# Optimization experiments

Measured on AMD Instinct MI355X. Metric: run time of the kernel, lower is better.

The kernel has to match this reference:

```python
import jax, jax.numpy as jnp
import numpy as np

T, B, D, H = 128, 64, 1024, 1024

def hard_sigmoid(x):
    # torch: clamp(x + 0.5, 0, 1)
    return jnp.clip(x + 0.5, 0.0, 1.0)

def hard_tanh(x):
    # torch F.hardtanh default: clamp(x, -1, 1)
    return jnp.clip(x, -1.0, 1.0)

def setup_inputs() -> dict:
    key = jax.random.key(0)
    k1, k2, k3 = jax.random.split(key, 3)
    scale = 1.0 / np.sqrt(H)
    x = jax.random.normal(k1, (T, B, D), dtype=jnp.float32)
    Wx = jax.random.normal(k2, (D, 4 * H), dtype=jnp.float32) * scale
    Wh = jax.random.normal(k3, (H, 4 * H), dtype=jnp.float32) * scale
    b = jnp.zeros((4 * H,), dtype=jnp.float32)
    return {"x": x, "Wx": Wx, "Wh": Wh, "b": b}

def reference(x, Wx, Wh, b):
    # Hard-LSTM cell unrolled over time (dim 0), state carried via lax.scan.
    Bsz = x.shape[1]
    Hd = Wh.shape[0]

    def step(carry, xt):
        h, c = carry
        gates = xt @ Wx + h @ Wh + b          # [B, 4H]
        i, f, g, o = jnp.split(gates, 4, axis=-1)
        i = hard_sigmoid(i)
        f = hard_sigmoid(f)
        g = hard_tanh(g)
        o = hard_sigmoid(o)
        c_new = f * c + i * g
        h_new = o * hard_tanh(c_new)
        return (h_new, c_new), h_new

    h0 = jnp.zeros((Bsz, Hd), dtype=x.dtype)
    c0 = jnp.zeros((Bsz, Hd), dtype=x.dtype)
    _, hs = jax.lax.scan(step, (h0, c0), x)   # hs: [T, B, H]
    return hs
```

## Files before the change

### kernel.cpp

```cpp
#include <hip/hip_runtime.h>

#define TT 128
#define BB 64
#define DD 1024
#define HH 1024
#define G4 4096
#define MM (TT*BB)
#define BH (BB*HH)

#define NWG 256

__device__ __forceinline__ float hsig(float x) {
    x += 0.5f;
    return fminf(fmaxf(x, 0.0f), 1.0f);
}
__device__ __forceinline__ float htanh(float x) {
    return fminf(fmaxf(x, -1.0f), 1.0f);
}

__global__ void zero_bar(unsigned* p) {
    p[threadIdx.x] = 0u;
}

__global__ __launch_bounds__(256) void gx_gemm(const float* __restrict__ X,
                                               const float* __restrict__ W,
                                               const float* __restrict__ bias,
                                               float* __restrict__ C) {
    __shared__ float As[16][132];
    __shared__ float Bs[16][132];

    const int tid = threadIdx.x;
    const int tx = tid & 15;
    const int ty = tid >> 4;
    const int m0 = blockIdx.y * 128;
    const int n0 = blockIdx.x * 128;

    float acc[8][8] = {};
    float4 ra[2], rb[2];

    #pragma unroll
    for (int i = 0; i < 2; ++i) {
        int f4 = tid + i * 256;
        ra[i] = *(const float4*)(X + (size_t)(m0 + (f4 >> 2)) * DD + (f4 & 3) * 4);
        rb[i] = *(const float4*)(W + (size_t)(f4 >> 5) * G4 + n0 + (f4 & 31) * 4);
    }

    for (int k0 = 0; k0 < DD; k0 += 16) {
        #pragma unroll
        for (int i = 0; i < 2; ++i) {
            int f4 = tid + i * 256;
            int mi = f4 >> 2, kq = f4 & 3;
            As[kq * 4 + 0][mi] = ra[i].x;
            As[kq * 4 + 1][mi] = ra[i].y;
            As[kq * 4 + 2][mi] = ra[i].z;
            As[kq * 4 + 3][mi] = ra[i].w;
            *(float4*)&Bs[f4 >> 5][(f4 & 31) * 4] = rb[i];
        }
        __syncthreads();

        const int kn = (k0 + 16 < DD) ? (k0 + 16) : k0;
        #pragma unroll
        for (int i = 0; i < 2; ++i) {
            int f4 = tid + i * 256;
            ra[i] = *(const float4*)(X + (size_t)(m0 + (f4 >> 2)) * DD + kn + (f4 & 3) * 4);
            rb[i] = *(const float4*)(W + (size_t)(kn + (f4 >> 5)) * G4 + n0 + (f4 & 31) * 4);
        }

        #pragma unroll
        for (int kk = 0; kk < 16; ++kk) {
            float ar[8], br[8];
            *(float4*)&ar[0] = *(const float4*)&As[kk][ty * 4];
            *(float4*)&ar[4] = *(const float4*)&As[kk][64 + ty * 4];
            *(float4*)&br[0] = *(const float4*)&Bs[kk][tx * 4];
            *(float4*)&br[4] = *(const float4*)&Bs[kk][64 + tx * 4];
            #pragma unroll
            for (int i = 0; i < 8; ++i)
                #pragma unroll
                for (int j = 0; j < 8; ++j)
                    acc[i][j] += ar[i] * br[j];
        }
        __syncthreads();
    }

    float bl[8];
    *(float4*)&bl[0] = *(const float4*)(bias + n0 + tx * 4);
    *(float4*)&bl[4] = *(const float4*)(bias + n0 + 64 + tx * 4);
    #pragma unroll
    for (int i = 0; i < 8; ++i) {
        int mrow = m0 + ty * 4 + (i & 3) + 64 * (i >> 2);
        float* crow = C + (size_t)mrow * G4 + n0;
        float4 o1, o2;
        o1.x = acc[i][0] + bl[0]; o1.y = acc[i][1] + bl[1];
        o1.z = acc[i][2] + bl[2]; o1.w = acc[i][3] + bl[3];
        o2.x = acc[i][4] + bl[4]; o2.y = acc[i][5] + bl[5];
        o2.z = acc[i][6] + bl[6]; o2.w = acc[i][7] + bl[7];
        *(float4*)(crow + tx * 4) = o1;
        *(float4*)(crow + 64 + tx * 4) = o2;
    }
}

__global__ __launch_bounds__(512) void lstm_persist(const float* __restrict__ Gx,
                                                    const float* __restrict__ Wh,
                                                    float* __restrict__ out,
                                                    unsigned* __restrict__ flags) {
    __shared__ float smem[16672];
    float* hs  = smem;
    float* red = smem;

    const int tid = threadIdx.x;
    const int btile = blockIdx.x >> 5;
    const int hct   = blockIdx.x & 31;
    const int b0 = btile * 8;

    const int kc = tid >> 4;
    const int tt = tid & 15;
    const int gate = tt >> 2;
    const int hq8  = (tt & 3) * 8;
    const float* wbase = Wh + (size_t)(kc * 32) * G4 + gate * HH + hct * 32 + hq8;

    const bool cell_act = (tid < 256);
    const int cb   = (tid >> 5) & 7;
    const int chcm = tid & 31;
    const size_t cell_g = (size_t)(b0 + cb) * G4 + hct * 32 + chcm;
    const size_t cell_h = (size_t)(b0 + cb) * HH + hct * 32 + chcm;
    float creg = 0.0f;

    const int half_id = cb >> 2;
    const int ridx = (cb & 3) * 8 + (chcm & 7);

    unsigned* gflags = flags + btile * 32;

    if (cell_act) {
        const float* gr = Gx + cell_g;
        float ii = hsig(gr[0]);
        float gv = htanh(gr[2 * HH]);
        float oo = hsig(gr[3 * HH]);
        creg = ii * gv;
        __hip_atomic_store(out + cell_h, oo * htanh(creg),
                           __ATOMIC_RELAXED, __HIP_MEMORY_SCOPE_AGENT);
    }
    asm volatile("s_waitcnt vmcnt(0)" ::: "memory");
    __syncthreads();
    if (tid == 0)
        __hip_atomic_store(gflags + hct, 1u, __ATOMIC_RELAXED,
                           __HIP_MEMORY_SCOPE_AGENT);

    for (int t = 1; t < TT; ++t) {
        float gi = 0.f, gf = 0.f, gg = 0.f, go = 0.f;
        if (cell_act) {
            const float* gr = Gx + (size_t)t * BB * G4 + cell_g;
            gi = gr[0];
            gf = gr[HH];
            gg = gr[2 * HH];
            go = gr[3 * HH];
        }

        if (tid < 32) {
            while (__hip_atomic_load(gflags + tid, __ATOMIC_RELAXED,
                                     __HIP_MEMORY_SCOPE_AGENT) < (unsigned)t)
                __builtin_amdgcn_s_sleep(1);
        }
        __syncthreads();

        const float* hprev = out + (size_t)(t - 1) * BH;
        #pragma unroll
        for (int i = 0; i < 16; ++i) {
            int idx = tid + i * 512;
            int bi = idx >> 10;
            int q  = idx & 1023;
            float v = __hip_atomic_load(hprev + (size_t)(b0 + bi) * HH + q,
                                        __ATOMIC_RELAXED, __HIP_MEMORY_SCOPE_AGENT);
            hs[bi * 1152 + (q >> 5) * 36 + (q & 31)] = v;
        }
        __syncthreads();

        float acc[8][8] = {};
        const float* wp = wbase;
        #pragma unroll 2
        for (int k4 = 0; k4 < 8; ++k4) {
            float4 hv[8];
            #pragma unroll
            for (int bi = 0; bi < 8; ++bi)
                hv[bi] = *(const float4*)&hs[bi * 1152 + kc * 36 + k4 * 4];
            #pragma unroll
            for (int j = 0; j < 4; ++j) {
                float4 w0 = *(const float4*)(wp);
                float4 w1 = *(const float4*)(wp + 4);
                wp += G4;
                #pragma unroll
                for (int bi = 0; bi < 8; ++bi) {
                    float h = (j == 0) ? hv[bi].x : (j == 1) ? hv[bi].y
                              : (j == 2) ? hv[bi].z : hv[bi].w;
                    acc[bi][0] += h * w0.x;
                    acc[bi][1] += h * w0.y;
                    acc[bi][2] += h * w0.z;
                    acc[bi][3] += h * w0.w;
                    acc[bi][4] += h * w1.x;
                    acc[bi][5] += h * w1.y;
                    acc[bi][6] += h * w1.z;
                    acc[bi][7] += h * w1.w;
                }
            }
        }
        __syncthreads();

        float gates[4] = {0.f, 0.f, 0.f, 0.f};
        #pragma unroll
        for (int half = 0; half < 2; ++half) {
            #pragma unroll
            for (int bi = 0; bi < 4; ++bi)
                #pragma unroll
                for (int j = 0; j < 8; ++j)
                    red[(size_t)(bi * 8 + j) * 521 + tid] = acc[half * 4 + bi][j];
            __syncthreads();
            if (cell_act && (half_id == half)) {
                #pragma unroll
                for (int g = 0; g < 4; ++g) {
                    const int wt = g * 4 + (chcm >> 3);
                    float s = 0.0f;
                    #pragma unroll
                    for (int k2 = 0; k2 < 32; ++k2)
                        s += red[(size_t)ridx * 521 + k2 * 16 + wt];
                    gates[g] = s;
                }
            }
            __syncthreads();
        }

        if (cell_act) {
            float ii = hsig(gi + gates[0]);
            float ff = hsig(gf + gates[1]);
            float gv = htanh(gg + gates[2]);
            float oo = hsig(go + gates[3]);
            creg = ff * creg + ii * gv;
            __hip_atomic_store(out + (size_t)t * BH + cell_h, oo * htanh(creg),
                               __ATOMIC_RELAXED, __HIP_MEMORY_SCOPE_AGENT);
        }
        asm volatile("s_waitcnt vmcnt(0)" ::: "memory");
        __syncthreads();
        if (tid == 0)
            __hip_atomic_store(gflags + hct, (unsigned)(t + 1),
                               __ATOMIC_RELAXED, __HIP_MEMORY_SCOPE_AGENT);
    }
}

extern "C" void kernel_launch(void* const* d_in, const int* in_sizes, int n_in,
                              void* d_out, int out_size, void* d_ws, size_t ws_size,
                              hipStream_t stream) {
    const float* x  = (const float*)d_in[0];
    const float* Wx = (const float*)d_in[1];
    const float* Wh = (const float*)d_in[2];
    const float* bs = (const float*)d_in[3];
    float* out = (float*)d_out;

    float* Gx = (float*)d_ws;
    unsigned* flags = (unsigned*)(Gx + (size_t)MM * G4);

    zero_bar<<<dim3(1), dim3(256), 0, stream>>>(flags);

    gx_gemm<<<dim3(G4 / 128, MM / 128), dim3(256), 0, stream>>>(x, Wx, bs, Gx);

    lstm_persist<<<dim3(NWG), dim3(512), 0, stream>>>(Gx, Wh, out, flags);
}
```

Measured before the change: 2.542 ms.

## Split recurrent LSTM across 512 workgroups with 16-column hidden tiles

```diff
diff --git a/kernel.cpp b/kernel.cpp
--- a/kernel.cpp
+++ b/kernel.cpp
@@ -8,7 +8,10 @@
 #define MM (TT*BB)
 #define BH (BB*HH)
 
-#define NWG 256
+#define NWG 512
+#define RPAD 520
+
+typedef float f32x4 __attribute__((ext_vector_type(4)));
 
 __device__ __forceinline__ float hsig(float x) {
     x += 0.5f;
@@ -99,36 +102,36 @@
     }
 }
 
-__global__ __launch_bounds__(512) void lstm_persist(const float* __restrict__ Gx,
-                                                    const float* __restrict__ Wh,
-                                                    float* __restrict__ out,
-                                                    unsigned* __restrict__ flags) {
-    __shared__ float smem[16672];
-    float* hs  = smem;
-    float* red = smem;
-
-    const int tid = threadIdx.x;
-    const int btile = blockIdx.x >> 5;
-    const int hct   = blockIdx.x & 31;
-    const int b0 = btile * 8;
-
-    const int kc = tid >> 4;
-    const int tt = tid & 15;
-    const int gate = tt >> 2;
-    const int hq8  = (tt & 3) * 8;
-    const float* wbase = Wh + (size_t)(kc * 32) * G4 + gate * HH + hct * 32 + hq8;
-
-    const bool cell_act = (tid < 256);
-    const int cb   = (tid >> 5) & 7;
-    const int chcm = tid & 31;
-    const size_t cell_g = (size_t)(b0 + cb) * G4 + hct * 32 + chcm;
-    const size_t cell_h = (size_t)(b0 + cb) * HH + hct * 32 + chcm;
+__global__ __launch_bounds__(512, 4) void lstm_persist(const float* __restrict__ Gx,
+                                                       const float* __restrict__ Wh,
+                                                       float* __restrict__ out,
+                                                       unsigned* __restrict__ flags) {
+    __shared__ float smem[16640 + 512];
+    float* hs   = smem;
+    float* red  = smem;
+    float* gsum = smem + 16640;
+
+    const int tid   = threadIdx.x;
+    const int btile = blockIdx.x >> 6;
+    const int hct   = blockIdx.x & 63;
+    const int b0  = btile * 8;
+    const int hc0 = hct * 16;
+
+    const int kc = tid >> 3;
+    const int tt = tid & 7;
+    const int gate_m = tt >> 1;
+    const int sub = (tt & 1) * 8;
+    const float* wbase = Wh + (size_t)(kc * 16) * G4 + gate_m * HH + hc0 + sub;
+    const int hbase = (kc >> 1) * 36 + (kc & 1) * 16;
+
+    const bool cell_act = (tid < 128);
+    const int cb  = tid >> 4;
+    const int chc = tid & 15;
+    const size_t cell_g = (size_t)(b0 + cb) * G4 + hc0 + chc;
+    const size_t cell_h = (size_t)(b0 + cb) * HH + hc0 + chc;
     float creg = 0.0f;
 
-    const int half_id = cb >> 2;
-    const int ridx = (cb & 3) * 8 + (chcm & 7);
-
-    unsigned* gflags = flags + btile * 32;
+    unsigned* gflags = flags + btile * 64;
 
     if (cell_act) {
         const float* gr = Gx + cell_g;
@@ -155,83 +158,104 @@
             go = gr[3 * HH];
         }
 
-        if (tid < 32) {
+        if (tid < 64) {
             while (__hip_atomic_load(gflags + tid, __ATOMIC_RELAXED,
                                      __HIP_MEMORY_SCOPE_AGENT) < (unsigned)t)
                 __builtin_amdgcn_s_sleep(1);
         }
         __syncthreads();
 
-        const float* hprev = out + (size_t)(t - 1) * BH;
-        #pragma unroll
-        for (int i = 0; i < 16; ++i) {
-            int idx = tid + i * 512;
-            int bi = idx >> 10;
-            int q  = idx & 1023;
-            float v = __hip_atomic_load(hprev + (size_t)(b0 + bi) * HH + q,
-                                        __ATOMIC_RELAXED, __HIP_MEMORY_SCOPE_AGENT);
-            hs[bi * 1152 + (q >> 5) * 36 + (q & 31)] = v;
+        {
+            const float* hprev = out + (size_t)(t - 1) * BH;
+            const float* sp[4];
+            int wbi[4], wq[4];
+            #pragma unroll
+            for (int i = 0; i < 4; ++i) {
+                int idx4 = tid + i * 512;
+                wbi[i] = idx4 >> 8;
+                wq[i]  = (idx4 & 255) * 4;
+                sp[i]  = hprev + (size_t)(b0 + wbi[i]) * HH + wq[i];
+            }
+            f32x4 v0, v1, v2, v3;
+            asm volatile(
+                "global_load_dwordx4 %0, %4, off sc0 sc1\n\t"
+                "global_load_dwordx4 %1, %5, off sc0 sc1\n\t"
+                "global_load_dwordx4 %2, %6, off sc0 sc1\n\t"
+                "global_load_dwordx4 %3, %7, off sc0 sc1\n\t"
+                "s_waitcnt vmcnt(0)"
+                : "=&v"(v0), "=&v"(v1), "=&v"(v2), "=&v"(v3)
+                : "v"(sp[0]), "v"(sp[1]), "v"(sp[2]), "v"(sp[3])
+                : "memory");
+            *(f32x4*)&hs[wbi[0] * 1152 + (wq[0] >> 5) * 36 + (wq[0] & 31)] = v0;
+            *(f32x4*)&hs[wbi[1] * 1152 + (wq[1] >> 5) * 36 + (wq[1] & 31)] = v1;
+            *(f32x4*)&hs[wbi[2] * 1152 + (wq[2] >> 5) * 36 + (wq[2] & 31)] = v2;
+            *(f32x4*)&hs[wbi[3] * 1152 + (wq[3] >> 5) * 36 + (wq[3] & 31)] = v3;
         }
         __syncthreads();
 
         float acc[8][8] = {};
         const float* wp = wbase;
         #pragma unroll 2
-        for (int k4 = 0; k4 < 8; ++k4) {
-            float4 hv[8];
+        for (int k4 = 0; k4 < 4; ++k4) {
+            f32x4 hv[8];
             #pragma unroll
             for (int bi = 0; bi < 8; ++bi)
-                hv[bi] = *(const float4*)&hs[bi * 1152 + kc * 36 + k4 * 4];
+                hv[bi] = *(const f32x4*)&hs[bi * 1152 + hbase + k4 * 4];
             #pragma unroll
             for (int j = 0; j < 4; ++j) {
-                float4 w0 = *(const float4*)(wp);
-                float4 w1 = *(const float4*)(wp + 4);
+                f32x4 w0 = *(const f32x4*)(wp);
+                f32x4 w1 = *(const f32x4*)(wp + 4);
                 wp += G4;
                 #pragma unroll
                 for (int bi = 0; bi < 8; ++bi) {
-                    float h = (j == 0) ? hv[bi].x : (j == 1) ? hv[bi].y
-                              : (j == 2) ? hv[bi].z : hv[bi].w;
-                    acc[bi][0] += h * w0.x;
-                    acc[bi][1] += h * w0.y;
-                    acc[bi][2] += h * w0.z;
-                    acc[bi][3] += h * w0.w;
-                    acc[bi][4] += h * w1.x;
-                    acc[bi][5] += h * w1.y;
-                    acc[bi][6] += h * w1.z;
-                    acc[bi][7] += h * w1.w;
+                    float h = hv[bi][j];
+                    acc[bi][0] += h * w0[0];
+                    acc[bi][1] += h * w0[1];
+                    acc[bi][2] += h * w0[2];
+                    acc[bi][3] += h * w0[3];
+                    acc[bi][4] += h * w1[0];
+                    acc[bi][5] += h * w1[1];
+                    acc[bi][6] += h * w1[2];
+                    acc[bi][7] += h * w1[3];
                 }
             }
         }
         __syncthreads();
 
-        float gates[4] = {0.f, 0.f, 0.f, 0.f};
-        #pragma unroll
-        for (int half = 0; half < 2; ++half) {
+        #pragma unroll
+        for (int round = 0; round < 2; ++round) {
             #pragma unroll
             for (int bi = 0; bi < 4; ++bi)
                 #pragma unroll
                 for (int j = 0; j < 8; ++j)
-                    red[(size_t)(bi * 8 + j) * 521 + tid] = acc[half * 4 + bi][j];
+                    red[(size_t)(bi * 8 + j) * RPAD + tid] = acc[round * 4 + bi][j];
             __syncthreads();
-            if (cell_act && (half_id == half)) {
-                #pragma unroll
-                for (int g = 0; g < 4; ++g) {
-                    const int wt = g * 4 + (chcm >> 3);
-                    float s = 0.0f;
-                    #pragma unroll
-                    for (int k2 = 0; k2 < 32; ++k2)
-                        s += red[(size_t)ridx * 521 + k2 * 16 + wt];
-                    gates[g] = s;
+            if ((tid >> 8) == round) {
+                const int r2  = tid & 255;
+                const int rb  = r2 >> 6;
+                const int gc  = r2 & 63;
+                const int rhc = gc & 15;
+                const int rtt = (gc >> 4) * 2 + (rhc >> 3);
+                const int vidx = rb * 8 + (rhc & 7);
+                const float* rp = red + (size_t)vidx * RPAD + rtt;
+                float s0 = 0.f, s1 = 0.f, s2 = 0.f, s3 = 0.f;
+                #pragma unroll
+                for (int k2 = 0; k2 < 64; k2 += 4) {
+                    s0 += rp[(k2 + 0) * 8];
+                    s1 += rp[(k2 + 1) * 8];
+                    s2 += rp[(k2 + 2) * 8];
+                    s3 += rp[(k2 + 3) * 8];
                 }
+                gsum[(round * 4 + rb) * 64 + gc] = (s0 + s1) + (s2 + s3);
             }
             __syncthreads();
         }
 
         if (cell_act) {
-            float ii = hsig(gi + gates[0]);
-            float ff = hsig(gf + gates[1]);
-            float gv = htanh(gg + gates[2]);
-            float oo = hsig(go + gates[3]);
+            float ii = hsig(gi + gsum[cb * 64 + chc]);
+            float ff = hsig(gf + gsum[cb * 64 + 16 + chc]);
+            float gv = htanh(gg + gsum[cb * 64 + 32 + chc]);
+            float oo = hsig(go + gsum[cb * 64 + 48 + chc]);
             creg = ff * creg + ii * gv;
             __hip_atomic_store(out + (size_t)t * BH + cell_h, oo * htanh(creg),
                                __ATOMIC_RELAXED, __HIP_MEMORY_SCOPE_AGENT);
@@ -256,7 +280,7 @@
     float* Gx = (float*)d_ws;
     unsigned* flags = (unsigned*)(Gx + (size_t)MM * G4);
 
-    zero_bar<<<dim3(1), dim3(256), 0, stream>>>(flags);
+    zero_bar<<<dim3(1), dim3(512), 0, stream>>>(flags);
 
     gx_gemm<<<dim3(G4 / 128, MM / 128), dim3(256), 0, stream>>>(x, Wx, bs, Gx);
 
```

New measurement: 5.749 ms. +126.1%, slower.
